# Optimization experiments

Hardware: AMD Instinct MI355X
Metric: run time of the kernel (lower is better)

Reference implementation:

```python
import jax, jax.numpy as jnp
import numpy as np

EPS = 1e-5

def _layernorm(x, gamma, beta):
    # LayerNormalization over last axis (channels), epsilon=1e-5
    mu = jnp.mean(x, axis=-1, keepdims=True)
    var = jnp.var(x, axis=-1, keepdims=True)
    return (x - mu) * jax.lax.rsqrt(var + EPS) * gamma + beta

def setup_inputs() -> dict:
    key = jax.random.key(0)
    ks = jax.random.split(key, 6)
    B, H, W, C = 8, 64, 64, 256
    std = 0.1  # NIN init_scale
    return {
        "x": jax.random.normal(ks[0], (B, H, W, C), dtype=jnp.float32),
        "ln_gamma": jnp.ones((C,), dtype=jnp.float32),
        "ln_beta": jnp.zeros((C,), dtype=jnp.float32),
        "wq": jax.random.normal(ks[1], (C, C), dtype=jnp.float32) * std,
        "bq": jnp.zeros((C,), dtype=jnp.float32),
        "wk": jax.random.normal(ks[2], (C, C), dtype=jnp.float32) * std,
        "bk": jnp.zeros((C,), dtype=jnp.float32),
        "wv": jax.random.normal(ks[3], (C, C), dtype=jnp.float32) * std,
        "bv": jnp.zeros((C,), dtype=jnp.float32),
        "wo": jax.random.normal(ks[4], (C, C), dtype=jnp.float32) * std,
        "bo": jnp.zeros((C,), dtype=jnp.float32),
    }

def reference(x, ln_gamma, ln_beta, wq, bq, wk, bk, wv, bv, wo, bo):
    B, H, W, C = x.shape
    h = _layernorm(x, ln_gamma, ln_beta)
    # 1x1 convs == per-pixel channel matmuls
    q = jnp.einsum('bhwc,cd->bhwd', h, wq) + bq
    k = jnp.einsum('bhwc,cd->bhwd', h, wk) + bk
    v = jnp.einsum('bhwc,cd->bhwd', h, wv) + bv
    scale = jnp.float32(C) ** -0.5
    # dense spatial attention over all H*W tokens
    w = jnp.einsum('bhwc,bijc->bhwij', q, k) * scale  # [B,H,W,H,W]
    w = jax.nn.softmax(w.reshape(B, H, W, H * W), axis=-1).reshape(B, H, W, H, W)
    h = jnp.einsum('bhwij,bijc->bhwc', w, v)
    h = jnp.einsum('bhwc,cd->bhwd', h, wo) + bo
    return x + h
```

## Files before the change

kernel.cpp:

```cpp
#include <hip/hip_runtime.h>
#include <stdint.h>

#define NB    8
#define NTOK  4096
#define TOK   32768
#define CDIM  256
#define BQ    128
#define BK    64
#define NT    (NTOK / BK)

#define KPITCH 264
#define VPITCH 68
#define KTILE_SH (BK * KPITCH)
#define VTILE_SH (CDIM * VPITCH)
#define KCH   33
#define VCH   34
#define TOTCH (KCH + VCH)

typedef __attribute__((ext_vector_type(8))) short bf16x8;
typedef __attribute__((ext_vector_type(4))) float f32x4;

#define SSCALE 0.09016844f

static __device__ __forceinline__ unsigned short f2bf(float f) {
    union { float f; unsigned u; } v; v.f = f;
    unsigned r = v.u + 0x7fffu + ((v.u >> 16) & 1u);
    return (unsigned short)(r >> 16);
}

static __device__ __forceinline__ void dma16(const unsigned short* g, unsigned short* l) {
    __builtin_amdgcn_global_load_lds(
        (const __attribute__((address_space(1))) unsigned int*)g,
        (__attribute__((address_space(3))) unsigned int*)l,
        16, 0, 0);
}

__global__ __launch_bounds__(256) void prep_kernel(
        const float* __restrict__ x,
        const float* __restrict__ gamma,
        const float* __restrict__ beta,
        const float* __restrict__ w0, const float* __restrict__ w1,
        const float* __restrict__ w2, const float* __restrict__ w3,
        unsigned short* __restrict__ h_bf,
        unsigned short* __restrict__ wt) {
    int bx = blockIdx.x;
    if (bx >= TOK / 4) {
        int id = bx - TOK / 4;
        int m = id >> 8, dd = id & 255;
        const float* src = (m == 0) ? w0 : (m == 1) ? w1 : (m == 2) ? w2 : w3;
        wt[m * (CDIM * CDIM) + dd * CDIM + threadIdx.x] = f2bf(src[threadIdx.x * CDIM + dd]);
        return;
    }
    int w = threadIdx.x >> 6;
    int lane = threadIdx.x & 63;
    int token = bx * 4 + w;
    const float4 xv = ((const float4*)(x + (size_t)token * CDIM))[lane];
    float s = xv.x + xv.y + xv.z + xv.w;
    #pragma unroll
    for (int off = 1; off < 64; off <<= 1) s += __shfl_xor(s, off, 64);
    float mean = s * (1.0f / 256.0f);
    float d0 = xv.x - mean, d1 = xv.y - mean, d2 = xv.z - mean, d3 = xv.w - mean;
    float ss = d0 * d0 + d1 * d1 + d2 * d2 + d3 * d3;
    #pragma unroll
    for (int off = 1; off < 64; off <<= 1) ss += __shfl_xor(ss, off, 64);
    float rstd = rsqrtf(ss * (1.0f / 256.0f) + 1e-5f);
    float4 g = ((const float4*)gamma)[lane];
    float4 b = ((const float4*)beta)[lane];
    ushort4 o;
    o.x = f2bf(d0 * rstd * g.x + b.x);
    o.y = f2bf(d1 * rstd * g.y + b.y);
    o.z = f2bf(d2 * rstd * g.z + b.z);
    o.w = f2bf(d3 * rstd * g.w + b.w);
    ((ushort4*)(h_bf + (size_t)token * CDIM))[lane] = o;
}

__global__ __launch_bounds__(128) void qkv_kernel(
        const unsigned short* __restrict__ h_bf,
        const unsigned short* __restrict__ wts,
        const float* __restrict__ bq,
        const float* __restrict__ bk,
        const float* __restrict__ bv,
        unsigned short* __restrict__ q_bf,
        unsigned short* __restrict__ k2,
        unsigned short* __restrict__ vt2) {
    __shared__ unsigned short VT[64][VPITCH];
    int tid = threadIdx.x;
    int w = tid >> 6, lane = tid & 63, quad = lane >> 4, l16 = lane & 15;
    int blk = blockIdx.x;
    int gy = blockIdx.y;
    int nt0 = gy * 4;
    int tok_base = blk * 64 + w * 32;

    bf16x8 afr[2][8];
    #pragma unroll
    for (int s = 0; s < 2; ++s)
        #pragma unroll
        for (int kk = 0; kk < 8; ++kk)
            afr[s][kk] = *(const bf16x8*)(h_bf + (size_t)(tok_base + s * 16 + l16) * CDIM + kk * 32 + quad * 8);

    {
        const unsigned short* wq_t = wts;
        #pragma unroll
        for (int ntl = 0; ntl < 4; ++ntl) {
            int nt = nt0 + ntl;
            f32x4 acc0 = {0.f, 0.f, 0.f, 0.f};
            f32x4 acc1 = {0.f, 0.f, 0.f, 0.f};
            #pragma unroll
            for (int kk = 0; kk < 8; ++kk) {
                bf16x8 bfr = *(const bf16x8*)(wq_t + (size_t)(nt * 16 + l16) * CDIM + kk * 32 + quad * 8);
                acc0 = __builtin_amdgcn_mfma_f32_16x16x32_bf16(bfr, afr[0][kk], acc0, 0, 0, 0);
                acc1 = __builtin_amdgcn_mfma_f32_16x16x32_bf16(bfr, afr[1][kk], acc1, 0, 0, 0);
            }
            int d0 = nt * 16 + quad * 4;
            float4 b4 = *(const float4*)(bq + d0);
            ushort4 o0, o1;
            o0.x = f2bf((acc0[0] + b4.x) * SSCALE); o0.y = f2bf((acc0[1] + b4.y) * SSCALE);
            o0.z = f2bf((acc0[2] + b4.z) * SSCALE); o0.w = f2bf((acc0[3] + b4.w) * SSCALE);
            o1.x = f2bf((acc1[0] + b4.x) * SSCALE); o1.y = f2bf((acc1[1] + b4.y) * SSCALE);
            o1.z = f2bf((acc1[2] + b4.z) * SSCALE); o1.w = f2bf((acc1[3] + b4.w) * SSCALE);
            *(ushort4*)(q_bf + (size_t)(tok_base + l16) * CDIM + d0)      = o0;
            *(ushort4*)(q_bf + (size_t)(tok_base + 16 + l16) * CDIM + d0) = o1;
        }
    }
    {
        const unsigned short* wk_t = wts + CDIM * CDIM;
        unsigned short* kdst = k2 + (size_t)blk * KTILE_SH;
        int key0 = w * 32 + l16;
        #pragma unroll
        for (int ntl = 0; ntl < 4; ++ntl) {
            int nt = nt0 + ntl;
            f32x4 acc0 = {0.f, 0.f, 0.f, 0.f};
            f32x4 acc1 = {0.f, 0.f, 0.f, 0.f};
            #pragma unroll
            for (int kk = 0; kk < 8; ++kk) {
                bf16x8 bfr = *(const bf16x8*)(wk_t + (size_t)(nt * 16 + l16) * CDIM + kk * 32 + quad * 8);
                acc0 = __builtin_amdgcn_mfma_f32_16x16x32_bf16(bfr, afr[0][kk], acc0, 0, 0, 0);
                acc1 = __builtin_amdgcn_mfma_f32_16x16x32_bf16(bfr, afr[1][kk], acc1, 0, 0, 0);
            }
            int d0 = nt * 16 + quad * 4;
            float4 b4 = *(const float4*)(bk + d0);
            ushort4 o0, o1;
            o0.x = f2bf(acc0[0] + b4.x); o0.y = f2bf(acc0[1] + b4.y);
            o0.z = f2bf(acc0[2] + b4.z); o0.w = f2bf(acc0[3] + b4.w);
            o1.x = f2bf(acc1[0] + b4.x); o1.y = f2bf(acc1[1] + b4.y);
            o1.z = f2bf(acc1[2] + b4.z); o1.w = f2bf(acc1[3] + b4.w);
            *(ushort4*)(kdst + (size_t)key0 * KPITCH + d0)        = o0;
            *(ushort4*)(kdst + (size_t)(key0 + 16) * KPITCH + d0) = o1;
        }
    }
    {
        const unsigned short* wv_t = wts + 2 * CDIM * CDIM;
        #pragma unroll
        for (int ntl = 0; ntl < 4; ++ntl) {
            int nt = nt0 + ntl;
            f32x4 acc0 = {0.f, 0.f, 0.f, 0.f};
            f32x4 acc1 = {0.f, 0.f, 0.f, 0.f};
            #pragma unroll
            for (int kk = 0; kk < 8; ++kk) {
                bf16x8 bfr = *(const bf16x8*)(wv_t + (size_t)(nt * 16 + l16) * CDIM + kk * 32 + quad * 8);
                acc0 = __builtin_amdgcn_mfma_f32_16x16x32_bf16(afr[0][kk], bfr, acc0, 0, 0, 0);
                acc1 = __builtin_amdgcn_mfma_f32_16x16x32_bf16(afr[1][kk], bfr, acc1, 0, 0, 0);
            }
            int d = nt * 16 + l16;
            float bb = bv[d];
            int dl = ntl * 16 + l16;
            #pragma unroll
            for (int r = 0; r < 4; ++r) {
                VT[dl][w * 32 + quad * 8 + r]     = f2bf(acc0[r] + bb);
                VT[dl][w * 32 + quad * 8 + 4 + r] = f2bf(acc1[r] + bb);
            }
        }
    }
    __syncthreads();
    const uint4* src = (const uint4*)(&VT[0][0]);
    uint4* dst = (uint4*)(vt2 + (size_t)blk * VTILE_SH + (size_t)gy * 64 * VPITCH);
    #pragma unroll
    for (int i = 0; i < 4; ++i)
        dst[i * 128 + tid] = src[i * 128 + tid];
    if (tid < 32) dst[512 + tid] = src[512 + tid];
}

#define DMA_TILE(KS, VS, ktn)                                                        \
    {                                                                                \
        const unsigned short* gk = k2 + (size_t)(b * NT + (ktn)) * KTILE_SH;         \
        const unsigned short* gv = vt2 + (size_t)(b * NT + (ktn)) * VTILE_SH;        \
        for (int c = w; c < TOTCH; c += 8) {                                         \
            if (c < KCH) dma16(gk + c * 512 + lane * 8, &KS[0][0] + c * 512);        \
            else dma16(gv + (c - KCH) * 512 + lane * 8, &VS[0][0] + (c - KCH) * 512);\
        }                                                                            \
    }

#define COMPUTE_TILE(KS, VS)                                                         \
    {                                                                                \
        f32x4 sfr[2][2];                                                             \
        _Pragma("unroll")                                                            \
        for (int nt = 0; nt < 2; ++nt) {                                             \
            f32x4 a0 = {0.f, 0.f, 0.f, 0.f};                                         \
            f32x4 a1 = {0.f, 0.f, 0.f, 0.f};                                         \
            _Pragma("unroll")                                                        \
            for (int kk = 0; kk < 8; ++kk) {                                         \
                bf16x8 kb = *(const bf16x8*)(&KS[kh * 32 + nt * 16 + l16][kk * 32 + quad * 8]); \
                a0 = __builtin_amdgcn_mfma_f32_16x16x32_bf16(kb, qfr[0][kk], a0, 0, 0, 0);      \
                a1 = __builtin_amdgcn_mfma_f32_16x16x32_bf16(kb, qfr[1][kk], a1, 0, 0, 0);      \
            }                                                                        \
            sfr[0][nt] = a0; sfr[1][nt] = a1;                                        \
        }                                                                            \
        int4 pwv[2];                                                                 \
        _Pragma("unroll")                                                            \
        for (int s = 0; s < 2; ++s) {                                                \
            unsigned pw[4];                                                          \
            _Pragma("unroll")                                                        \
            for (int nt = 0; nt < 2; ++nt)                                           \
                _Pragma("unroll")                                                    \
                for (int h = 0; h < 2; ++h) {                                        \
                    float plo = exp2f(sfr[s][nt][2 * h]);                            \
                    float phi = exp2f(sfr[s][nt][2 * h + 1]);                        \
                    lacc[s] += plo + phi;                                            \
                    pw[nt * 2 + h] = (__float_as_uint(plo) >> 16)                    \
                                   | (__float_as_uint(phi) & 0xffff0000u);           \
                }                                                                    \
            pwv[s] = make_int4(pw[0], pw[1], pw[2], pw[3]);                          \
        }                                                                            \
        bf16x8 pfr0 = *(bf16x8*)&pwv[0];                                             \
        bf16x8 pfr1 = *(bf16x8*)&pwv[1];                                             \
        _Pragma("unroll")                                                            \
        for (int nt2 = 0; nt2 < 16; ++nt2) {                                         \
            bf16x8 vb = *(const bf16x8*)(&VS[nt2 * 16 + l16][kh * 32 + quad * 8]);   \
            O[0][nt2] = __builtin_amdgcn_mfma_f32_16x16x32_bf16(pfr0, vb, O[0][nt2], 0, 0, 0);  \
            O[1][nt2] = __builtin_amdgcn_mfma_f32_16x16x32_bf16(pfr1, vb, O[1][nt2], 0, 0, 0);  \
        }                                                                            \
    }

__global__ __launch_bounds__(512, 2) void flash_kernel(
        const unsigned short* __restrict__ q_bf,
        const unsigned short* __restrict__ k2,
        const unsigned short* __restrict__ vt2,
        const unsigned short* __restrict__ wo_t,
        const float* __restrict__ bo,
        const float* __restrict__ x,
        float* __restrict__ out) {
    __shared__ unsigned short Ks0[BK][KPITCH];
    __shared__ unsigned short Ks1[BK][KPITCH];
    __shared__ unsigned short Vs0[CDIM][VPITCH];
    __shared__ unsigned short Vs1[CDIM][VPITCH];
    __shared__ float sLbuf[512];

    int tid = threadIdx.x;
    int w = tid >> 6, lane = tid & 63, quad = lane >> 4, l16 = lane & 15;
    int kh = w >> 2;
    int wq = w & 3;
    int bid = blockIdx.x;
    int b = bid & 7;
    int qtile = bid >> 3;
    int qrow = qtile * BQ + wq * 32;
    const size_t bbase = (size_t)b * NTOK * CDIM;

    bf16x8 qfr[2][8];
    #pragma unroll
    for (int s = 0; s < 2; ++s)
        #pragma unroll
        for (int kk = 0; kk < 8; ++kk)
            qfr[s][kk] = *(const bf16x8*)(q_bf + bbase + (size_t)(qrow + s * 16 + l16) * CDIM + kk * 32 + quad * 8);

    f32x4 O[2][16];
    #pragma unroll
    for (int s = 0; s < 2; ++s)
        #pragma unroll
        for (int i = 0; i < 16; ++i) O[s][i] = (f32x4){0.f, 0.f, 0.f, 0.f};
    float lacc[2] = {0.f, 0.f};

    DMA_TILE(Ks0, Vs0, 0);
    __syncthreads();

    for (int kt2 = 0; kt2 < NT; kt2 += 2) {
        DMA_TILE(Ks1, Vs1, kt2 + 1);
        COMPUTE_TILE(Ks0, Vs0);
        __syncthreads();
        if (kt2 + 2 < NT) DMA_TILE(Ks0, Vs0, kt2 + 2);
        COMPUTE_TILE(Ks1, Vs1);
        __syncthreads();
    }

    float* sO = (wq == 0) ? (float*)&Ks0[0][0] : (wq == 1) ? (float*)&Ks1[0][0]
              : (wq == 2) ? (float*)&Vs0[0][0] : (float*)&Vs1[0][0];
    float* sL = sLbuf + wq * 128;

    if (kh == 1) {
        #pragma unroll
        for (int s = 0; s < 2; ++s) {
            #pragma unroll
            for (int nt2 = 0; nt2 < 16; ++nt2)
                #pragma unroll
                for (int r = 0; r < 4; ++r)
                    sO[((s * 16 + nt2) * 4 + r) * 64 + lane] = O[s][nt2][r];
            sL[s * 64 + lane] = lacc[s];
        }
    }
    __syncthreads();
    if (kh == 0) {
        float lr[2][4];
        #pragma unroll
        for (int s = 0; s < 2; ++s) {
            float ls = lacc[s] + sL[s * 64 + lane];
            ls += __shfl_xor(ls, 16, 64);
            ls += __shfl_xor(ls, 32, 64);
            float li = 1.0f / ls;
            #pragma unroll
            for (int r = 0; r < 4; ++r)
                lr[s][r] = __shfl(li, quad * 4 + r, 64);
        }
        #pragma unroll
        for (int s = 0; s < 2; ++s)
            #pragma unroll
            for (int nt2 = 0; nt2 < 16; ++nt2)
                #pragma unroll
                for (int r = 0; r < 4; ++r)
                    O[s][nt2][r] = (O[s][nt2][r] + sO[((s * 16 + nt2) * 4 + r) * 64 + lane]) * lr[s][r];
    }
    __syncthreads();

    if (kh == 0) {
        if (wq < 2) {
            #pragma unroll
            for (int s = 0; s < 2; ++s)
                #pragma unroll
                for (int nt2 = 0; nt2 < 16; ++nt2)
                    #pragma unroll
                    for (int r = 0; r < 4; ++r)
                        Ks0[(wq & 1) * 32 + s * 16 + quad * 4 + r][nt2 * 16 + l16] = f2bf(O[s][nt2][r]);
        } else {
            #pragma unroll
            for (int s = 0; s < 2; ++s)
                #pragma unroll
                for (int nt2 = 0; nt2 < 16; ++nt2)
                    #pragma unroll
                    for (int r = 0; r < 4; ++r)
                        Ks1[(wq & 1) * 32 + s * 16 + quad * 4 + r][nt2 * 16 + l16] = f2bf(O[s][nt2][r]);
        }
    }
    __syncthreads();

    {
        bf16x8 wfr[2][8];
        #pragma unroll
        for (int t = 0; t < 2; ++t)
            #pragma unroll
            for (int kk = 0; kk < 8; ++kk)
                wfr[t][kk] = *(const bf16x8*)(wo_t + (size_t)((w * 2 + t) * 16 + l16) * CDIM + kk * 32 + quad * 8);
        float bb0 = bo[(w * 2 + 0) * 16 + l16];
        float bb1 = bo[(w * 2 + 1) * 16 + l16];
        int tok0 = qtile * BQ;
        #pragma unroll
        for (int rg = 0; rg < 8; ++rg) {
            bf16x8 afr2[8];
            #pragma unroll
            for (int kk = 0; kk < 8; ++kk)
                afr2[kk] = (rg < 4)
                    ? *(const bf16x8*)(&Ks0[rg * 16 + l16][kk * 32 + quad * 8])
                    : *(const bf16x8*)(&Ks1[(rg - 4) * 16 + l16][kk * 32 + quad * 8]);
            f32x4 acc0 = {0.f, 0.f, 0.f, 0.f};
            f32x4 acc1 = {0.f, 0.f, 0.f, 0.f};
            #pragma unroll
            for (int kk = 0; kk < 8; ++kk) {
                acc0 = __builtin_amdgcn_mfma_f32_16x16x32_bf16(afr2[kk], wfr[0][kk], acc0, 0, 0, 0);
                acc1 = __builtin_amdgcn_mfma_f32_16x16x32_bf16(afr2[kk], wfr[1][kk], acc1, 0, 0, 0);
            }
            #pragma unroll
            for (int r = 0; r < 4; ++r) {
                size_t idx = bbase + (size_t)(tok0 + rg * 16 + quad * 4 + r) * CDIM;
                size_t i0 = idx + (w * 2 + 0) * 16 + l16;
                size_t i1 = idx + (w * 2 + 1) * 16 + l16;
                out[i0] = x[i0] + acc0[r] + bb0;
                out[i1] = x[i1] + acc1[r] + bb1;
            }
        }
    }
}

extern "C" void kernel_launch(void* const* d_in, const int* in_sizes, int n_in,
                              void* d_out, int out_size, void* d_ws, size_t ws_size,
                              hipStream_t stream) {
    const float* x     = (const float*)d_in[0];
    const float* gamma = (const float*)d_in[1];
    const float* beta  = (const float*)d_in[2];
    const float* wq    = (const float*)d_in[3];
    const float* bq    = (const float*)d_in[4];
    const float* wk    = (const float*)d_in[5];
    const float* bk    = (const float*)d_in[6];
    const float* wv    = (const float*)d_in[7];
    const float* bv    = (const float*)d_in[8];
    const float* wo    = (const float*)d_in[9];
    const float* bo    = (const float*)d_in[10];
    float* out = (float*)d_out;

    char* ws = (char*)d_ws;
    unsigned short* h_bf = (unsigned short*)(ws);
    unsigned short* q_bf = (unsigned short*)(ws + 16777216);
    unsigned short* k2   = (unsigned short*)(ws + 33554432);
    unsigned short* vt2  = (unsigned short*)(ws + 50855936);
    unsigned short* wt   = (unsigned short*)(ws + 68681728);

    prep_kernel<<<TOK / 4 + 1024, 256, 0, stream>>>(x, gamma, beta, wq, wk, wv, wo, h_bf, wt);
    qkv_kernel<<<dim3(TOK / 64, 4), 128, 0, stream>>>(h_bf, wt, bq, bk, bv, q_bf, k2, vt2);
    flash_kernel<<<(NTOK / BQ) * NB, 512, 0, stream>>>(
        q_bf, k2, vt2, wt + 3 * (CDIM * CDIM), bo, x, out);
}
```

Measured before the change: 339.6 us.

## Fuse LayerNorm into QKV projection and raise wave priority around MFMA blocks

LayerNorm moves out of the prep kernel and into the QKV kernel, which now reads fp32 x directly, computes mean and variance with shuffles, and builds bf16 A fragments in registers. This removes the h_bf intermediate write and read, and weight transposition becomes its own small kernel. Because the QKV grid has 4 column blocks per token group, each token's LayerNorm is now recomputed 4 times, and variance is computed as E[x^2]-mean^2, which is less numerically stable. The flash kernel also wraps its MFMA sections in s_setprio so matrix work is favoured over the exp and softmax phases.

```diff
diff --git a/kernel.cpp b/kernel.cpp
--- a/kernel.cpp
+++ b/kernel.cpp
@@ -35,47 +35,20 @@
         16, 0, 0);
 }
 
-__global__ __launch_bounds__(256) void prep_kernel(
+__global__ __launch_bounds__(256) void wtrans_kernel(
+        const float* __restrict__ w0, const float* __restrict__ w1,
+        const float* __restrict__ w2, const float* __restrict__ w3,
+        unsigned short* __restrict__ wt) {
+    int id = blockIdx.x;
+    int m = id >> 8, dd = id & 255;
+    const float* src = (m == 0) ? w0 : (m == 1) ? w1 : (m == 2) ? w2 : w3;
+    wt[m * (CDIM * CDIM) + dd * CDIM + threadIdx.x] = f2bf(src[threadIdx.x * CDIM + dd]);
+}
+
+__global__ __launch_bounds__(128) void qkv_kernel(
         const float* __restrict__ x,
         const float* __restrict__ gamma,
         const float* __restrict__ beta,
-        const float* __restrict__ w0, const float* __restrict__ w1,
-        const float* __restrict__ w2, const float* __restrict__ w3,
-        unsigned short* __restrict__ h_bf,
-        unsigned short* __restrict__ wt) {
-    int bx = blockIdx.x;
-    if (bx >= TOK / 4) {
-        int id = bx - TOK / 4;
-        int m = id >> 8, dd = id & 255;
-        const float* src = (m == 0) ? w0 : (m == 1) ? w1 : (m == 2) ? w2 : w3;
-        wt[m * (CDIM * CDIM) + dd * CDIM + threadIdx.x] = f2bf(src[threadIdx.x * CDIM + dd]);
-        return;
-    }
-    int w = threadIdx.x >> 6;
-    int lane = threadIdx.x & 63;
-    int token = bx * 4 + w;
-    const float4 xv = ((const float4*)(x + (size_t)token * CDIM))[lane];
-    float s = xv.x + xv.y + xv.z + xv.w;
-    #pragma unroll
-    for (int off = 1; off < 64; off <<= 1) s += __shfl_xor(s, off, 64);
-    float mean = s * (1.0f / 256.0f);
-    float d0 = xv.x - mean, d1 = xv.y - mean, d2 = xv.z - mean, d3 = xv.w - mean;
-    float ss = d0 * d0 + d1 * d1 + d2 * d2 + d3 * d3;
-    #pragma unroll
-    for (int off = 1; off < 64; off <<= 1) ss += __shfl_xor(ss, off, 64);
-    float rstd = rsqrtf(ss * (1.0f / 256.0f) + 1e-5f);
-    float4 g = ((const float4*)gamma)[lane];
-    float4 b = ((const float4*)beta)[lane];
-    ushort4 o;
-    o.x = f2bf(d0 * rstd * g.x + b.x);
-    o.y = f2bf(d1 * rstd * g.y + b.y);
-    o.z = f2bf(d2 * rstd * g.z + b.z);
-    o.w = f2bf(d3 * rstd * g.w + b.w);
-    ((ushort4*)(h_bf + (size_t)token * CDIM))[lane] = o;
-}
-
-__global__ __launch_bounds__(128) void qkv_kernel(
-        const unsigned short* __restrict__ h_bf,
         const unsigned short* __restrict__ wts,
         const float* __restrict__ bq,
         const float* __restrict__ bk,
@@ -93,10 +66,42 @@
 
     bf16x8 afr[2][8];
     #pragma unroll
-    for (int s = 0; s < 2; ++s)
-        #pragma unroll
-        for (int kk = 0; kk < 8; ++kk)
-            afr[s][kk] = *(const bf16x8*)(h_bf + (size_t)(tok_base + s * 16 + l16) * CDIM + kk * 32 + quad * 8);
+    for (int s = 0; s < 2; ++s) {
+        const float* xr = x + (size_t)(tok_base + s * 16 + l16) * CDIM;
+        float s1 = 0.f, s2 = 0.f;
+        #pragma unroll
+        for (int kk = 0; kk < 8; ++kk) {
+            float4 a = *(const float4*)(xr + kk * 32 + quad * 8);
+            float4 c = *(const float4*)(xr + kk * 32 + quad * 8 + 4);
+            s1 += a.x + a.y + a.z + a.w + c.x + c.y + c.z + c.w;
+            s2 += a.x * a.x + a.y * a.y + a.z * a.z + a.w * a.w
+                + c.x * c.x + c.y * c.y + c.z * c.z + c.w * c.w;
+        }
+        s1 += __shfl_xor(s1, 16, 64); s1 += __shfl_xor(s1, 32, 64);
+        s2 += __shfl_xor(s2, 16, 64); s2 += __shfl_xor(s2, 32, 64);
+        float mean = s1 * (1.0f / 256.0f);
+        float var  = s2 * (1.0f / 256.0f) - mean * mean;
+        float rstd = rsqrtf(var + 1e-5f);
+        #pragma unroll
+        for (int kk = 0; kk < 8; ++kk) {
+            float4 a  = *(const float4*)(xr + kk * 32 + quad * 8);
+            float4 c  = *(const float4*)(xr + kk * 32 + quad * 8 + 4);
+            float4 g0 = *(const float4*)(gamma + kk * 32 + quad * 8);
+            float4 g1 = *(const float4*)(gamma + kk * 32 + quad * 8 + 4);
+            float4 b0 = *(const float4*)(beta + kk * 32 + quad * 8);
+            float4 b1 = *(const float4*)(beta + kk * 32 + quad * 8 + 4);
+            union { bf16x8 v; unsigned short u[8]; } pk;
+            pk.u[0] = f2bf((a.x - mean) * rstd * g0.x + b0.x);
+            pk.u[1] = f2bf((a.y - mean) * rstd * g0.y + b0.y);
+            pk.u[2] = f2bf((a.z - mean) * rstd * g0.z + b0.z);
+            pk.u[3] = f2bf((a.w - mean) * rstd * g0.w + b0.w);
+            pk.u[4] = f2bf((c.x - mean) * rstd * g1.x + b1.x);
+            pk.u[5] = f2bf((c.y - mean) * rstd * g1.y + b1.y);
+            pk.u[6] = f2bf((c.z - mean) * rstd * g1.z + b1.z);
+            pk.u[7] = f2bf((c.w - mean) * rstd * g1.w + b1.w);
+            afr[s][kk] = pk.v;
+        }
+    }
 
     {
         const unsigned short* wq_t = wts;
@@ -193,6 +198,7 @@
 #define COMPUTE_TILE(KS, VS)                                                         \
     {                                                                                \
         f32x4 sfr[2][2];                                                             \
+        __builtin_amdgcn_s_setprio(1);                                               \
         _Pragma("unroll")                                                            \
         for (int nt = 0; nt < 2; ++nt) {                                             \
             f32x4 a0 = {0.f, 0.f, 0.f, 0.f};                                         \
@@ -205,6 +211,7 @@
             }                                                                        \
             sfr[0][nt] = a0; sfr[1][nt] = a1;                                        \
         }                                                                            \
+        __builtin_amdgcn_s_setprio(0);                                               \
         int4 pwv[2];                                                                 \
         _Pragma("unroll")                                                            \
         for (int s = 0; s < 2; ++s) {                                                \
@@ -223,12 +230,14 @@
         }                                                                            \
         bf16x8 pfr0 = *(bf16x8*)&pwv[0];                                             \
         bf16x8 pfr1 = *(bf16x8*)&pwv[1];                                             \
+        __builtin_amdgcn_s_setprio(1);                                               \
         _Pragma("unroll")                                                            \
         for (int nt2 = 0; nt2 < 16; ++nt2) {                                         \
             bf16x8 vb = *(const bf16x8*)(&VS[nt2 * 16 + l16][kh * 32 + quad * 8]);   \
             O[0][nt2] = __builtin_amdgcn_mfma_f32_16x16x32_bf16(pfr0, vb, O[0][nt2], 0, 0, 0);  \
             O[1][nt2] = __builtin_amdgcn_mfma_f32_16x16x32_bf16(pfr1, vb, O[1][nt2], 0, 0, 0);  \
         }                                                                            \
+        __builtin_amdgcn_s_setprio(0);                                               \
     }
 
 __global__ __launch_bounds__(512, 2) void flash_kernel(
@@ -394,14 +403,13 @@
     float* out = (float*)d_out;
 
     char* ws = (char*)d_ws;
-    unsigned short* h_bf = (unsigned short*)(ws);
     unsigned short* q_bf = (unsigned short*)(ws + 16777216);
     unsigned short* k2   = (unsigned short*)(ws + 33554432);
     unsigned short* vt2  = (unsigned short*)(ws + 50855936);
     unsigned short* wt   = (unsigned short*)(ws + 68681728);
 
-    prep_kernel<<<TOK / 4 + 1024, 256, 0, stream>>>(x, gamma, beta, wq, wk, wv, wo, h_bf, wt);
-    qkv_kernel<<<dim3(TOK / 64, 4), 128, 0, stream>>>(h_bf, wt, bq, bk, bv, q_bf, k2, vt2);
+    wtrans_kernel<<<1024, 256, 0, stream>>>(wq, wk, wv, wo, wt);
+    qkv_kernel<<<dim3(TOK / 64, 4), 128, 0, stream>>>(x, gamma, beta, wt, bq, bk, bv, q_bf, k2, vt2);
     flash_kernel<<<(NTOK / BQ) * NB, 512, 0, stream>>>(
         q_bf, k2, vt2, wt + 3 * (CDIM * CDIM), bo, x, out);
 }
```

After: 375.3 us. 10.5% more time.
